# Kernel tuning notes

Hardware: AMD Instinct MI355X
Metric: run time of the kernel (lower is better)

Reference implementation:

```python
import jax, jax.numpy as jnp
import numpy as np

N_NODES = 100000
N_EDGES = 1600000
D_IN = 32
D_OUT = 32


def setup_inputs() -> dict:
    key = jax.random.key(0)
    k1, k2, k3 = jax.random.split(key, 3)
    x = jax.random.normal(k1, (N_NODES, D_IN), dtype=jnp.float32)
    edge_index = jax.random.randint(k2, (2, N_EDGES), 0, N_NODES, dtype=jnp.int64)
    # nn.Linear weight: [out_channels, in_channels]
    W = jax.random.normal(k3, (D_OUT, D_IN), dtype=jnp.float32) * (1.0 / np.sqrt(D_IN))
    return {"x": x, "edge_index": edge_index, "W": W}


def reference(x, edge_index, W):
    src, dst = edge_index[0], edge_index[1]
    # gather source features and scatter-add to destination nodes
    agg = jax.ops.segment_sum(x[src], dst, num_segments=x.shape[0])  # [N, D_IN]
    # linear (no bias): agg @ W.T
    return agg @ W.T
```

## Files before the change

kernel.cpp:

```cpp
#include <hip/hip_runtime.h>

#define N_NODES 100000
#define N_EDGES 1600000
#define D 32
#define Q8 256.0f
#define INV_Q8 (1.0f / 256.0f)
#define ROWS_PER_BLOCK 64
#define XS_STRIDE 36
#define NTILES ((N_NODES + ROWS_PER_BLOCK - 1) / ROWS_PER_BLOCK)
#define POISON64 0xAAAAAAAAAAAAAAAAULL
#define POISON32 0xAAAAAAAAu

#define BKT_NODES 256
#define NB ((N_NODES + BKT_NODES - 1) / BKT_NODES)
#define CAPB 8192
#define EPB 4096
#define K1_EPT (EPB / 256)
#define K1_BLOCKS ((N_EDGES + EPB - 1) / EPB)
#define K2_THREADS 512
#define QCAP 2048
#define MAX_WPT 12

#define GCUR_OFF 0
#define BUF_OFF  4096
#define YPK_OFF  (BUF_OFF + (size_t)NB * CAPB * 4)
#define WS_NEEDED (YPK_OFF + (size_t)N_NODES * 8 * 8)

__device__ __forceinline__ void decode4(unsigned long long s, float* o) {
    short v0 = (short)(s & 0xFFFF);
    s = (s >> 16) + (unsigned long long)(v0 < 0 ? 1 : 0);
    short v1 = (short)(s & 0xFFFF);
    s = (s >> 16) + (unsigned long long)(v1 < 0 ? 1 : 0);
    short v2 = (short)(s & 0xFFFF);
    s = (s >> 16) + (unsigned long long)(v2 < 0 ? 1 : 0);
    short v3 = (short)(s & 0xFFFF);
    o[0] = (float)v0 * INV_Q8;
    o[1] = (float)v1 * INV_Q8;
    o[2] = (float)v2 * INV_Q8;
    o[3] = (float)v3 * INV_Q8;
}

__global__ __launch_bounds__(256) void gcn_pack_bucket_kernel(
    const float4* __restrict__ x4,
    const float* __restrict__ W,
    const int* __restrict__ src,
    const int* __restrict__ dst,
    unsigned long long* __restrict__ ypk,
    unsigned int* __restrict__ gcur,
    unsigned int* __restrict__ buf) {
    __shared__ float xs[ROWS_PER_BLOCK * XS_STRIDE];
    __shared__ float Wt[D * D];
    __shared__ unsigned int cnt[NB];
    __shared__ unsigned int base[NB];
    int t = threadIdx.x;
    int b = blockIdx.x;

    if (b < NTILES) {
#pragma unroll
        for (int i = t; i < D * D; i += 256) {
            int o = i >> 5, k = i & 31;
            Wt[k * D + o] = W[i];
        }
        int row0 = b * ROWS_PER_BLOCK;
        int r = t >> 2;
        int c = t & 3;
        int grow = row0 + r;
        if (grow < N_NODES) {
            float4 v0 = x4[(size_t)grow * 8 + c * 2];
            float4 v1 = x4[(size_t)grow * 8 + c * 2 + 1];
            float* dp = &xs[r * XS_STRIDE + c * 8];
            dp[0] = v0.x; dp[1] = v0.y; dp[2] = v0.z; dp[3] = v0.w;
            dp[4] = v1.x; dp[5] = v1.y; dp[6] = v1.z; dp[7] = v1.w;
        }
        __syncthreads();
        if (grow >= N_NODES) return;

        int q = t & 3;
        float acc[8];
#pragma unroll
        for (int j = 0; j < 8; ++j) acc[j] = 0.f;
#pragma unroll
        for (int k = 0; k < D; ++k) {
            float v = xs[r * XS_STRIDE + k];
#pragma unroll
            for (int j = 0; j < 8; ++j) acc[j] += v * Wt[k * D + q * 8 + j];
        }
        long long a[8];
#pragma unroll
        for (int j = 0; j < 8; ++j)
            a[j] = (long long)__float2int_rn(acc[j] * Q8);
        unsigned long long p0 = (unsigned long long)(
            a[0] + (a[1] << 16) + (a[2] << 32) + (a[3] << 48));
        unsigned long long p1 = (unsigned long long)(
            a[4] + (a[5] << 16) + (a[6] << 32) + (a[7] << 48));
        ulonglong2* op = (ulonglong2*)(ypk + (size_t)grow * 8 + q * 2);
        *op = make_ulonglong2(p0, p1);
        return;
    }

    for (int j = t; j < NB; j += 256) cnt[j] = 0;
    __syncthreads();

    int e0 = (b - NTILES) * EPB;
    int s[K1_EPT], bkt[K1_EPT];
    unsigned int rank[K1_EPT], word[K1_EPT];
    bool ok[K1_EPT];
#pragma unroll
    for (int i = 0; i < K1_EPT; ++i) {
        int e = e0 + i * 256 + t;
        ok[i] = e < N_EDGES;
        int dd = 0;
        if (ok[i]) { s[i] = src[e]; dd = dst[e]; }
        bkt[i] = dd >> 8;
        word[i] = (unsigned int)s[i] | ((unsigned int)(dd & 255) << 17);
    }
#pragma unroll
    for (int i = 0; i < K1_EPT; ++i)
        if (ok[i]) rank[i] = atomicAdd(&cnt[bkt[i]], 1u);
    __syncthreads();

    for (int j = t; j < NB; j += 256) {
        unsigned int c = cnt[j];
        base[j] = c ? (atomicAdd(&gcur[j], c) - POISON32) : 0u;
    }
    __syncthreads();

#pragma unroll
    for (int i = 0; i < K1_EPT; ++i) {
        if (ok[i]) {
            unsigned int idx = base[bkt[i]] + rank[i];
            if (idx < CAPB)
                buf[(size_t)bkt[i] * CAPB + idx] = word[i];
        }
    }
}

__global__ __launch_bounds__(K2_THREADS) void gcn_sort_agg_kernel(
    const unsigned int* __restrict__ gcur,
    const unsigned int* __restrict__ buf,
    const unsigned long long* __restrict__ ypk,
    float* __restrict__ out) {
    __shared__ unsigned int sorted[QCAP];
    __shared__ unsigned int cnt[64];
    __shared__ unsigned int pfx[65];
    int t = threadIdx.x;
    int bq = blockIdx.x;
    int b = bq >> 2;
    int q = bq & 3;

    if (t < 64) cnt[t] = 0;
    __syncthreads();

    unsigned int cntb = gcur[b] - POISON32;
    if (cntb > 6144u) cntb = 6144u;
    const unsigned int* bb = buf + (size_t)b * CAPB;

    unsigned int w[MAX_WPT], rk[MAX_WPT];
    bool ok[MAX_WPT];
#pragma unroll
    for (int i = 0; i < MAX_WPT; ++i) {
        unsigned int g = (unsigned int)t + (unsigned int)i * K2_THREADS;
        ok[i] = (g < cntb);
        w[i] = ok[i] ? bb[g] : 0u;
        ok[i] = ok[i] && (((w[i] >> 23) & 3u) == (unsigned int)q);
    }
#pragma unroll
    for (int i = 0; i < MAX_WPT; ++i)
        if (ok[i]) rk[i] = atomicAdd(&cnt[(w[i] >> 17) & 63u], 1u);
    __syncthreads();

    if (t < 64) {
        unsigned int c = cnt[t];
        unsigned int v = c;
#pragma unroll
        for (int off = 1; off < 64; off <<= 1) {
            unsigned int u = __shfl_up(v, off, 64);
            if (t >= off) v += u;
        }
        pfx[t] = v - c;
        if (t == 63) pfx[64] = v;
    }
    __syncthreads();

#pragma unroll
    for (int i = 0; i < MAX_WPT; ++i) {
        if (ok[i]) {
            unsigned int idx = pfx[(w[i] >> 17) & 63u] + rk[i];
            if (idx < QCAP) sorted[idx] = w[i];
        }
    }
    __syncthreads();

    int r = t >> 3;
    int f4 = t & 7;
    unsigned int beg = pfx[r];
    unsigned int end = pfx[r + 1];
    unsigned long long sum = 0;
    unsigned int k = beg;
    for (; k + 8 <= end; k += 8) {
        unsigned int w0 = sorted[k],     w1 = sorted[k + 1];
        unsigned int w2 = sorted[k + 2], w3 = sorted[k + 3];
        unsigned int w4 = sorted[k + 4], w5 = sorted[k + 5];
        unsigned int w6 = sorted[k + 6], w7 = sorted[k + 7];
        unsigned long long y0 = ypk[(size_t)(w0 & 0x1FFFF) * 8 + f4];
        unsigned long long y1 = ypk[(size_t)(w1 & 0x1FFFF) * 8 + f4];
        unsigned long long y2 = ypk[(size_t)(w2 & 0x1FFFF) * 8 + f4];
        unsigned long long y3 = ypk[(size_t)(w3 & 0x1FFFF) * 8 + f4];
        unsigned long long y4 = ypk[(size_t)(w4 & 0x1FFFF) * 8 + f4];
        unsigned long long y5 = ypk[(size_t)(w5 & 0x1FFFF) * 8 + f4];
        unsigned long long y6 = ypk[(size_t)(w6 & 0x1FFFF) * 8 + f4];
        unsigned long long y7 = ypk[(size_t)(w7 & 0x1FFFF) * 8 + f4];
        sum += (y0 + y1) + (y2 + y3) + ((y4 + y5) + (y6 + y7));
    }
    for (; k < end; ++k)
        sum += ypk[(size_t)(sorted[k] & 0x1FFFF) * 8 + f4];

    int grow = (b << 8) + (q << 6) + r;
    if (grow < N_NODES) {
        float o4[4];
        decode4(sum, o4);
        *(float4*)(out + (size_t)grow * D + f4 * 4) =
            make_float4(o4[0], o4[1], o4[2], o4[3]);
    }
}


__global__ __launch_bounds__(256) void gcn_scatter_q_kernel(
    const int* __restrict__ src,
    const int* __restrict__ dst,
    const float4* __restrict__ x4,
    unsigned long long* __restrict__ agg) {
    int gid = blockIdx.x * 256 + threadIdx.x;
    int e = gid >> 3;
    int f4 = gid & 7;
    if (e >= N_EDGES) return;
    int s = src[e];
    int dd = dst[e];
    float4 v = x4[(size_t)s * 8 + f4];
    long long a0 = (long long)__float2int_rn(v.x * Q8);
    long long a1 = (long long)__float2int_rn(v.y * Q8);
    long long a2 = (long long)__float2int_rn(v.z * Q8);
    long long a3 = (long long)__float2int_rn(v.w * Q8);
    unsigned long long p =
        (unsigned long long)(a0 + (a1 << 16) + (a2 << 32) + (a3 << 48));
    atomicAdd(&agg[(size_t)dd * 8 + f4], p);
}

__global__ __launch_bounds__(256) void gcn_matmul_kernel(
    const unsigned long long* __restrict__ agg,
    const float* __restrict__ W,
    float* __restrict__ out) {
    __shared__ float xs[ROWS_PER_BLOCK * XS_STRIDE];
    __shared__ float Wt[D * D];
    int t = threadIdx.x;
    int b = blockIdx.x;

#pragma unroll
    for (int i = t; i < D * D; i += 256) {
        int o = i >> 5, k = i & 31;
        Wt[k * D + o] = W[i];
    }

    int row0 = b * ROWS_PER_BLOCK;
    {
        int r = t >> 2;
        int c = t & 3;
        int grow = row0 + r;
        if (grow < N_NODES) {
            const unsigned long long* rp = agg + (size_t)grow * 8 + c * 2;
            unsigned long long s0 = rp[0] - POISON64;
            unsigned long long s1 = rp[1] - POISON64;
            float* dstp = &xs[r * XS_STRIDE + c * 8];
            decode4(s0, dstp);
            decode4(s1, dstp + 4);
        }
    }
    __syncthreads();

    int r = t >> 2;
    int q = t & 3;
    int grow = row0 + r;
    if (grow >= N_NODES) return;

    float acc8[8];
#pragma unroll
    for (int j = 0; j < 8; ++j) acc8[j] = 0.f;
#pragma unroll
    for (int k = 0; k < D; ++k) {
        float v = xs[r * XS_STRIDE + k];
#pragma unroll
        for (int j = 0; j < 8; ++j) acc8[j] += v * Wt[k * D + q * 8 + j];
    }
    float4* op = (float4*)(out + (size_t)grow * D + q * 8);
    op[0] = make_float4(acc8[0], acc8[1], acc8[2], acc8[3]);
    op[1] = make_float4(acc8[4], acc8[5], acc8[6], acc8[7]);
}

extern "C" void kernel_launch(void* const* d_in, const int* in_sizes, int n_in,
                              void* d_out, int out_size, void* d_ws, size_t ws_size,
                              hipStream_t stream) {
    const float* x = (const float*)d_in[0];
    const int* edge_index = (const int*)d_in[1];
    const float* W = (const float*)d_in[2];
    float* out = (float*)d_out;

    const int* src = edge_index;
    const int* dst = edge_index + N_EDGES;

    char* ws = (char*)d_ws;

    if (ws_size >= WS_NEEDED) {
        unsigned int* gcur = (unsigned int*)(ws + GCUR_OFF);
        unsigned int* buf = (unsigned int*)(ws + BUF_OFF);
        unsigned long long* ypk = (unsigned long long*)(ws + YPK_OFF);

        gcn_pack_bucket_kernel<<<NTILES + K1_BLOCKS, 256, 0, stream>>>(
            (const float4*)x, W, src, dst, ypk, gcur, buf);
        gcn_sort_agg_kernel<<<NB * 4, K2_THREADS, 0, stream>>>(
            gcur, buf, ypk, out);
    } else {
        unsigned long long* agg = (unsigned long long*)ws;
        gcn_scatter_q_kernel<<<(N_EDGES * 8) / 256, 256, 0, stream>>>(
            src, dst, (const float4*)x, agg);
        gcn_matmul_kernel<<<NTILES, 256, 0, stream>>>(agg, W, out);
    }
}
```

Baseline: 119.6 us.

## Fuse bucketing, transform and sort-aggregate into one cooperative kernel with grid sync

Merges the pack/bucket kernel and the sort-aggregate kernel into a single cooperative launch of 512 persistent blocks. Each block first buckets a slice of edges, then computes and quantizes rows of x·W into a grid-strided set of tiles, and after a grid-wide sync it loops over the bucket quarters to sort and aggregate. This removes the second kernel launch and the inter-kernel gap. The cost is a grid barrier, fewer resident blocks with persistent loops, and a higher register and shared-memory footprint per block. The old two-kernel path remains as a fallback if the cooperative launch fails.

```diff
diff --git a/kernel.cpp b/kernel.cpp
--- a/kernel.cpp
+++ b/kernel.cpp
@@ -1,4 +1,7 @@
 #include <hip/hip_runtime.h>
+#include <hip/hip_cooperative_groups.h>
+
+namespace cg = cooperative_groups;
 
 #define N_NODES 100000
 #define N_EDGES 1600000
@@ -20,6 +23,10 @@
 #define K2_THREADS 512
 #define QCAP 2048
 #define MAX_WPT 12
+
+#define FUSE_BLOCKS 512
+#define FUSE_THREADS 512
+#define EPT2 (EPB / FUSE_THREADS)
 
 #define GCUR_OFF 0
 #define BUF_OFF  4096
@@ -40,120 +47,13 @@
     o[3] = (float)v3 * INV_Q8;
 }
 
-__global__ __launch_bounds__(256) void gcn_pack_bucket_kernel(
-    const float4* __restrict__ x4,
-    const float* __restrict__ W,
-    const int* __restrict__ src,
-    const int* __restrict__ dst,
-    unsigned long long* __restrict__ ypk,
-    unsigned int* __restrict__ gcur,
-    unsigned int* __restrict__ buf) {
-    __shared__ float xs[ROWS_PER_BLOCK * XS_STRIDE];
-    __shared__ float Wt[D * D];
-    __shared__ unsigned int cnt[NB];
-    __shared__ unsigned int base[NB];
+__device__ __forceinline__ void quarter_sort_agg(
+    int b, int q, unsigned int cntb, const unsigned int* __restrict__ bb,
+    const unsigned long long* __restrict__ ypk, float* __restrict__ out,
+    unsigned int* sorted, unsigned int* cnt, unsigned int* pfx) {
     int t = threadIdx.x;
-    int b = blockIdx.x;
-
-    if (b < NTILES) {
-#pragma unroll
-        for (int i = t; i < D * D; i += 256) {
-            int o = i >> 5, k = i & 31;
-            Wt[k * D + o] = W[i];
-        }
-        int row0 = b * ROWS_PER_BLOCK;
-        int r = t >> 2;
-        int c = t & 3;
-        int grow = row0 + r;
-        if (grow < N_NODES) {
-            float4 v0 = x4[(size_t)grow * 8 + c * 2];
-            float4 v1 = x4[(size_t)grow * 8 + c * 2 + 1];
-            float* dp = &xs[r * XS_STRIDE + c * 8];
-            dp[0] = v0.x; dp[1] = v0.y; dp[2] = v0.z; dp[3] = v0.w;
-            dp[4] = v1.x; dp[5] = v1.y; dp[6] = v1.z; dp[7] = v1.w;
-        }
-        __syncthreads();
-        if (grow >= N_NODES) return;
-
-        int q = t & 3;
-        float acc[8];
-#pragma unroll
-        for (int j = 0; j < 8; ++j) acc[j] = 0.f;
-#pragma unroll
-        for (int k = 0; k < D; ++k) {
-            float v = xs[r * XS_STRIDE + k];
-#pragma unroll
-            for (int j = 0; j < 8; ++j) acc[j] += v * Wt[k * D + q * 8 + j];
-        }
-        long long a[8];
-#pragma unroll
-        for (int j = 0; j < 8; ++j)
-            a[j] = (long long)__float2int_rn(acc[j] * Q8);
-        unsigned long long p0 = (unsigned long long)(
-            a[0] + (a[1] << 16) + (a[2] << 32) + (a[3] << 48));
-        unsigned long long p1 = (unsigned long long)(
-            a[4] + (a[5] << 16) + (a[6] << 32) + (a[7] << 48));
-        ulonglong2* op = (ulonglong2*)(ypk + (size_t)grow * 8 + q * 2);
-        *op = make_ulonglong2(p0, p1);
-        return;
-    }
-
-    for (int j = t; j < NB; j += 256) cnt[j] = 0;
-    __syncthreads();
-
-    int e0 = (b - NTILES) * EPB;
-    int s[K1_EPT], bkt[K1_EPT];
-    unsigned int rank[K1_EPT], word[K1_EPT];
-    bool ok[K1_EPT];
-#pragma unroll
-    for (int i = 0; i < K1_EPT; ++i) {
-        int e = e0 + i * 256 + t;
-        ok[i] = e < N_EDGES;
-        int dd = 0;
-        if (ok[i]) { s[i] = src[e]; dd = dst[e]; }
-        bkt[i] = dd >> 8;
-        word[i] = (unsigned int)s[i] | ((unsigned int)(dd & 255) << 17);
-    }
-#pragma unroll
-    for (int i = 0; i < K1_EPT; ++i)
-        if (ok[i]) rank[i] = atomicAdd(&cnt[bkt[i]], 1u);
-    __syncthreads();
-
-    for (int j = t; j < NB; j += 256) {
-        unsigned int c = cnt[j];
-        base[j] = c ? (atomicAdd(&gcur[j], c) - POISON32) : 0u;
-    }
-    __syncthreads();
-
-#pragma unroll
-    for (int i = 0; i < K1_EPT; ++i) {
-        if (ok[i]) {
-            unsigned int idx = base[bkt[i]] + rank[i];
-            if (idx < CAPB)
-                buf[(size_t)bkt[i] * CAPB + idx] = word[i];
-        }
-    }
-}
-
-__global__ __launch_bounds__(K2_THREADS) void gcn_sort_agg_kernel(
-    const unsigned int* __restrict__ gcur,
-    const unsigned int* __restrict__ buf,
-    const unsigned long long* __restrict__ ypk,
-    float* __restrict__ out) {
-    __shared__ unsigned int sorted[QCAP];
-    __shared__ unsigned int cnt[64];
-    __shared__ unsigned int pfx[65];
-    int t = threadIdx.x;
-    int bq = blockIdx.x;
-    int b = bq >> 2;
-    int q = bq & 3;
-
     if (t < 64) cnt[t] = 0;
     __syncthreads();
-
-    unsigned int cntb = gcur[b] - POISON32;
-    if (cntb > 6144u) cntb = 6144u;
-    const unsigned int* bb = buf + (size_t)b * CAPB;
 
     unsigned int w[MAX_WPT], rk[MAX_WPT];
     bool ok[MAX_WPT];
@@ -222,6 +122,221 @@
         *(float4*)(out + (size_t)grow * D + f4 * 4) =
             make_float4(o4[0], o4[1], o4[2], o4[3]);
     }
+    __syncthreads();
+}
+
+__global__ __launch_bounds__(FUSE_THREADS, 4) void gcn_fused_kernel(
+    const float4* __restrict__ x4, const float* __restrict__ W,
+    const int* __restrict__ src, const int* __restrict__ dst,
+    unsigned long long* __restrict__ ypk, unsigned int* __restrict__ gcur,
+    unsigned int* __restrict__ buf, float* __restrict__ out) {
+    __shared__ float Wt[D * D];
+    __shared__ float xs[64 * XS_STRIDE];
+    __shared__ unsigned int cnt1[NB];
+    __shared__ unsigned int base1[NB];
+    __shared__ unsigned int sorted[QCAP];
+    __shared__ unsigned int cnt2[64];
+    __shared__ unsigned int pfx[65];
+    int t = threadIdx.x;
+    int b = blockIdx.x;
+    int nblk = gridDim.x;
+
+    for (int i = t; i < D * D; i += FUSE_THREADS) {
+        int o = i >> 5, k = i & 31;
+        Wt[k * D + o] = W[i];
+    }
+
+    if (b < K1_BLOCKS) {
+        for (int j = t; j < NB; j += FUSE_THREADS) cnt1[j] = 0;
+        __syncthreads();
+        int e0 = b * EPB;
+        int s[EPT2], bkt[EPT2];
+        unsigned int rank[EPT2], word[EPT2];
+        bool ok[EPT2];
+#pragma unroll
+        for (int i = 0; i < EPT2; ++i) {
+            int e = e0 + i * FUSE_THREADS + t;
+            ok[i] = e < N_EDGES;
+            int dd = 0;
+            if (ok[i]) { s[i] = src[e]; dd = dst[e]; }
+            bkt[i] = dd >> 8;
+            word[i] = (unsigned int)s[i] | ((unsigned int)(dd & 255) << 17);
+        }
+#pragma unroll
+        for (int i = 0; i < EPT2; ++i)
+            if (ok[i]) rank[i] = atomicAdd(&cnt1[bkt[i]], 1u);
+        __syncthreads();
+        if (t < NB) {
+            unsigned int c = cnt1[t];
+            base1[t] = c ? (atomicAdd(&gcur[t], c) - POISON32) : 0u;
+        }
+        __syncthreads();
+#pragma unroll
+        for (int i = 0; i < EPT2; ++i) {
+            if (ok[i]) {
+                unsigned int idx = base1[bkt[i]] + rank[i];
+                if (idx < CAPB) buf[(size_t)bkt[i] * CAPB + idx] = word[i];
+            }
+        }
+    }
+    __syncthreads();
+
+    int tb = (b >= K1_BLOCKS) ? (b - K1_BLOCKS) : (b + (nblk - K1_BLOCKS));
+    for (int tile = tb; tile < NTILES; tile += nblk) {
+        int row0 = tile * ROWS_PER_BLOCK;
+        int r = t >> 3;
+        int h = t & 7;
+        int grow = row0 + r;
+        if (grow < N_NODES) {
+            float4 v = x4[(size_t)grow * 8 + h];
+            float* dp = &xs[r * XS_STRIDE + h * 4];
+            dp[0] = v.x; dp[1] = v.y; dp[2] = v.z; dp[3] = v.w;
+        }
+        __syncthreads();
+        if (grow < N_NODES) {
+            float acc[4];
+#pragma unroll
+            for (int j = 0; j < 4; ++j) acc[j] = 0.f;
+#pragma unroll
+            for (int k = 0; k < D; ++k) {
+                float v = xs[r * XS_STRIDE + k];
+#pragma unroll
+                for (int j = 0; j < 4; ++j) acc[j] += v * Wt[k * D + h * 4 + j];
+            }
+            long long a0 = (long long)__float2int_rn(acc[0] * Q8);
+            long long a1 = (long long)__float2int_rn(acc[1] * Q8);
+            long long a2 = (long long)__float2int_rn(acc[2] * Q8);
+            long long a3 = (long long)__float2int_rn(acc[3] * Q8);
+            ypk[(size_t)grow * 8 + h] = (unsigned long long)(
+                a0 + (a1 << 16) + (a2 << 32) + (a3 << 48));
+        }
+        __syncthreads();
+    }
+
+    cg::this_grid().sync();
+
+    for (int qq = b; qq < NB * 4; qq += nblk) {
+        int bb_ = qq >> 2, q = qq & 3;
+        unsigned int cntb = __hip_atomic_load(&gcur[bb_], __ATOMIC_RELAXED,
+                                              __HIP_MEMORY_SCOPE_AGENT) -
+                            POISON32;
+        if (cntb > 6144u) cntb = 6144u;
+        quarter_sort_agg(bb_, q, cntb, buf + (size_t)bb_ * CAPB, ypk, out,
+                         sorted, cnt2, pfx);
+    }
+}
+
+
+__global__ __launch_bounds__(256) void gcn_pack_bucket_kernel(
+    const float4* __restrict__ x4,
+    const float* __restrict__ W,
+    const int* __restrict__ src,
+    const int* __restrict__ dst,
+    unsigned long long* __restrict__ ypk,
+    unsigned int* __restrict__ gcur,
+    unsigned int* __restrict__ buf) {
+    __shared__ float xs[ROWS_PER_BLOCK * XS_STRIDE];
+    __shared__ float Wt[D * D];
+    __shared__ unsigned int cnt[NB];
+    __shared__ unsigned int base[NB];
+    int t = threadIdx.x;
+    int b = blockIdx.x;
+
+    if (b < NTILES) {
+#pragma unroll
+        for (int i = t; i < D * D; i += 256) {
+            int o = i >> 5, k = i & 31;
+            Wt[k * D + o] = W[i];
+        }
+        int row0 = b * ROWS_PER_BLOCK;
+        int r = t >> 2;
+        int c = t & 3;
+        int grow = row0 + r;
+        if (grow < N_NODES) {
+            float4 v0 = x4[(size_t)grow * 8 + c * 2];
+            float4 v1 = x4[(size_t)grow * 8 + c * 2 + 1];
+            float* dp = &xs[r * XS_STRIDE + c * 8];
+            dp[0] = v0.x; dp[1] = v0.y; dp[2] = v0.z; dp[3] = v0.w;
+            dp[4] = v1.x; dp[5] = v1.y; dp[6] = v1.z; dp[7] = v1.w;
+        }
+        __syncthreads();
+        if (grow >= N_NODES) return;
+
+        int q = t & 3;
+        float acc[8];
+#pragma unroll
+        for (int j = 0; j < 8; ++j) acc[j] = 0.f;
+#pragma unroll
+        for (int k = 0; k < D; ++k) {
+            float v = xs[r * XS_STRIDE + k];
+#pragma unroll
+            for (int j = 0; j < 8; ++j) acc[j] += v * Wt[k * D + q * 8 + j];
+        }
+        long long a[8];
+#pragma unroll
+        for (int j = 0; j < 8; ++j)
+            a[j] = (long long)__float2int_rn(acc[j] * Q8);
+        unsigned long long p0 = (unsigned long long)(
+            a[0] + (a[1] << 16) + (a[2] << 32) + (a[3] << 48));
+        unsigned long long p1 = (unsigned long long)(
+            a[4] + (a[5] << 16) + (a[6] << 32) + (a[7] << 48));
+        ulonglong2* op = (ulonglong2*)(ypk + (size_t)grow * 8 + q * 2);
+        *op = make_ulonglong2(p0, p1);
+        return;
+    }
+
+    for (int j = t; j < NB; j += 256) cnt[j] = 0;
+    __syncthreads();
+
+    int e0 = (b - NTILES) * EPB;
+    int s[K1_EPT], bkt[K1_EPT];
+    unsigned int rank[K1_EPT], word[K1_EPT];
+    bool ok[K1_EPT];
+#pragma unroll
+    for (int i = 0; i < K1_EPT; ++i) {
+        int e = e0 + i * 256 + t;
+        ok[i] = e < N_EDGES;
+        int dd = 0;
+        if (ok[i]) { s[i] = src[e]; dd = dst[e]; }
+        bkt[i] = dd >> 8;
+        word[i] = (unsigned int)s[i] | ((unsigned int)(dd & 255) << 17);
+    }
+#pragma unroll
+    for (int i = 0; i < K1_EPT; ++i)
+        if (ok[i]) rank[i] = atomicAdd(&cnt[bkt[i]], 1u);
+    __syncthreads();
+
+    for (int j = t; j < NB; j += 256) {
+        unsigned int c = cnt[j];
+        base[j] = c ? (atomicAdd(&gcur[j], c) - POISON32) : 0u;
+    }
+    __syncthreads();
+
+#pragma unroll
+    for (int i = 0; i < K1_EPT; ++i) {
+        if (ok[i]) {
+            unsigned int idx = base[bkt[i]] + rank[i];
+            if (idx < CAPB)
+                buf[(size_t)bkt[i] * CAPB + idx] = word[i];
+        }
+    }
+}
+
+__global__ __launch_bounds__(K2_THREADS) void gcn_sort_agg_kernel(
+    const unsigned int* __restrict__ gcur,
+    const unsigned int* __restrict__ buf,
+    const unsigned long long* __restrict__ ypk,
+    float* __restrict__ out) {
+    __shared__ unsigned int sorted[QCAP];
+    __shared__ unsigned int cnt[64];
+    __shared__ unsigned int pfx[65];
+    int bq = blockIdx.x;
+    int b = bq >> 2;
+    int q = bq & 3;
+    unsigned int cntb = gcur[b] - POISON32;
+    if (cntb > 6144u) cntb = 6144u;
+    quarter_sort_agg(b, q, cntb, buf + (size_t)b * CAPB, ypk, out,
+                     sorted, cnt, pfx);
 }
 
 
@@ -314,10 +429,27 @@
         unsigned int* buf = (unsigned int*)(ws + BUF_OFF);
         unsigned long long* ypk = (unsigned long long*)(ws + YPK_OFF);
 
-        gcn_pack_bucket_kernel<<<NTILES + K1_BLOCKS, 256, 0, stream>>>(
-            (const float4*)x, W, src, dst, ypk, gcur, buf);
-        gcn_sort_agg_kernel<<<NB * 4, K2_THREADS, 0, stream>>>(
-            gcur, buf, ypk, out);
+        const float4* x4p = (const float4*)x;
+        const float* Wp = W;
+        const int* srcp = src;
+        const int* dstp = dst;
+        unsigned long long* ypkp = ypk;
+        unsigned int* gcurp = gcur;
+        unsigned int* bufp = buf;
+        float* outp = out;
+        void* kargs[] = {(void*)&x4p,  (void*)&Wp,    (void*)&srcp,
+                         (void*)&dstp, (void*)&ypkp,  (void*)&gcurp,
+                         (void*)&bufp, (void*)&outp};
+        hipError_t cerr = hipLaunchCooperativeKernel(
+            (const void*)gcn_fused_kernel, dim3(FUSE_BLOCKS),
+            dim3(FUSE_THREADS), kargs, 0, stream);
+        if (cerr != hipSuccess) {
+            (void)hipGetLastError();
+            gcn_pack_bucket_kernel<<<NTILES + K1_BLOCKS, 256, 0, stream>>>(
+                (const float4*)x, W, src, dst, ypk, gcur, buf);
+            gcn_sort_agg_kernel<<<NB * 4, K2_THREADS, 0, stream>>>(
+                gcur, buf, ypk, out);
+        }
     } else {
         unsigned long long* agg = (unsigned long long*)ws;
         gcn_scatter_q_kernel<<<(N_EDGES * 8) / 256, 256, 0, stream>>>(
```

New measurement: 209.1 us. +74.9%, slower.

## Split packed projected features into two planes and aggregate each half separately

Applied to the files above, without the earlier changes.

The packed fixed-point projected features are stored as two feature planes of 16 columns each instead of one 32-column row. Aggregation now runs as two launches, one per plane, and each block covers 128 destination rows with 4 threads per row. Each pass gathers from a table half the size, which should improve cache hit rates on the random source gathers. The cost is one extra launch, and every bucket has to be re-read and re-sorted in each pass.

```diff
diff --git a/kernel.cpp b/kernel.cpp
--- a/kernel.cpp
+++ b/kernel.cpp
@@ -18,13 +18,14 @@
 #define K1_EPT (EPB / 256)
 #define K1_BLOCKS ((N_EDGES + EPB - 1) / EPB)
 #define K2_THREADS 512
-#define QCAP 2048
+#define HCAP 4096
 #define MAX_WPT 12
 
 #define GCUR_OFF 0
 #define BUF_OFF  4096
 #define YPK_OFF  (BUF_OFF + (size_t)NB * CAPB * 4)
-#define WS_NEEDED (YPK_OFF + (size_t)N_NODES * 8 * 8)
+#define PLANE_U64 ((size_t)N_NODES * 4)
+#define WS_NEEDED (YPK_OFF + 2 * PLANE_U64 * 8)
 
 __device__ __forceinline__ void decode4(unsigned long long s, float* o) {
     short v0 = (short)(s & 0xFFFF);
@@ -45,7 +46,8 @@
     const float* __restrict__ W,
     const int* __restrict__ src,
     const int* __restrict__ dst,
-    unsigned long long* __restrict__ ypk,
+    unsigned long long* __restrict__ ylo,
+    unsigned long long* __restrict__ yhi,
     unsigned int* __restrict__ gcur,
     unsigned int* __restrict__ buf) {
     __shared__ float xs[ROWS_PER_BLOCK * XS_STRIDE];
@@ -93,7 +95,9 @@
             a[0] + (a[1] << 16) + (a[2] << 32) + (a[3] << 48));
         unsigned long long p1 = (unsigned long long)(
             a[4] + (a[5] << 16) + (a[6] << 32) + (a[7] << 48));
-        ulonglong2* op = (ulonglong2*)(ypk + (size_t)grow * 8 + q * 2);
+        unsigned long long* plane = (q < 2) ? ylo : yhi;
+        ulonglong2* op =
+            (ulonglong2*)(plane + (size_t)grow * 4 + (q & 1) * 2);
         *op = make_ulonglong2(p0, p1);
         return;
     }
@@ -135,20 +139,22 @@
     }
 }
 
-__global__ __launch_bounds__(K2_THREADS) void gcn_sort_agg_kernel(
+template <int PLANE>
+__global__ __launch_bounds__(K2_THREADS) void gcn_sort_agg_half_kernel(
     const unsigned int* __restrict__ gcur,
     const unsigned int* __restrict__ buf,
-    const unsigned long long* __restrict__ ypk,
+    const unsigned long long* __restrict__ ypl,
     float* __restrict__ out) {
-    __shared__ unsigned int sorted[QCAP];
-    __shared__ unsigned int cnt[64];
-    __shared__ unsigned int pfx[65];
+    __shared__ unsigned int sorted[HCAP];
+    __shared__ unsigned int cnt[128];
+    __shared__ unsigned int pfx[129];
+    __shared__ unsigned int wtot[2];
     int t = threadIdx.x;
-    int bq = blockIdx.x;
-    int b = bq >> 2;
-    int q = bq & 3;
-
-    if (t < 64) cnt[t] = 0;
+    int bh = blockIdx.x;
+    int b = bh >> 1;
+    int h = bh & 1;
+
+    if (t < 128) cnt[t] = 0;
     __syncthreads();
 
     unsigned int cntb = gcur[b] - POISON32;
@@ -162,37 +168,43 @@
         unsigned int g = (unsigned int)t + (unsigned int)i * K2_THREADS;
         ok[i] = (g < cntb);
         w[i] = ok[i] ? bb[g] : 0u;
-        ok[i] = ok[i] && (((w[i] >> 23) & 3u) == (unsigned int)q);
+        ok[i] = ok[i] && (((w[i] >> 24) & 1u) == (unsigned int)h);
     }
 #pragma unroll
     for (int i = 0; i < MAX_WPT; ++i)
-        if (ok[i]) rk[i] = atomicAdd(&cnt[(w[i] >> 17) & 63u], 1u);
-    __syncthreads();
-
-    if (t < 64) {
-        unsigned int c = cnt[t];
-        unsigned int v = c;
+        if (ok[i]) rk[i] = atomicAdd(&cnt[(w[i] >> 17) & 127u], 1u);
+    __syncthreads();
+
+    unsigned int v = 0, c = 0;
+    if (t < 128) {
+        c = cnt[t];
+        v = c;
 #pragma unroll
         for (int off = 1; off < 64; off <<= 1) {
             unsigned int u = __shfl_up(v, off, 64);
-            if (t >= off) v += u;
-        }
-        pfx[t] = v - c;
-        if (t == 63) pfx[64] = v;
+            if ((t & 63) >= off) v += u;
+        }
+        if ((t & 63) == 63) wtot[t >> 6] = v;
+    }
+    __syncthreads();
+    if (t < 128) {
+        unsigned int add = (t >= 64) ? wtot[0] : 0u;
+        pfx[t] = v - c + add;
+        if (t == 127) pfx[128] = v + add;
     }
     __syncthreads();
 
 #pragma unroll
     for (int i = 0; i < MAX_WPT; ++i) {
         if (ok[i]) {
-            unsigned int idx = pfx[(w[i] >> 17) & 63u] + rk[i];
-            if (idx < QCAP) sorted[idx] = w[i];
-        }
-    }
-    __syncthreads();
-
-    int r = t >> 3;
-    int f4 = t & 7;
+            unsigned int idx = pfx[(w[i] >> 17) & 127u] + rk[i];
+            if (idx < HCAP) sorted[idx] = w[i];
+        }
+    }
+    __syncthreads();
+
+    int r = t >> 2;
+    int f4 = t & 3;
     unsigned int beg = pfx[r];
     unsigned int end = pfx[r + 1];
     unsigned long long sum = 0;
@@ -202,24 +214,24 @@
         unsigned int w2 = sorted[k + 2], w3 = sorted[k + 3];
         unsigned int w4 = sorted[k + 4], w5 = sorted[k + 5];
         unsigned int w6 = sorted[k + 6], w7 = sorted[k + 7];
-        unsigned long long y0 = ypk[(size_t)(w0 & 0x1FFFF) * 8 + f4];
-        unsigned long long y1 = ypk[(size_t)(w1 & 0x1FFFF) * 8 + f4];
-        unsigned long long y2 = ypk[(size_t)(w2 & 0x1FFFF) * 8 + f4];
-        unsigned long long y3 = ypk[(size_t)(w3 & 0x1FFFF) * 8 + f4];
-        unsigned long long y4 = ypk[(size_t)(w4 & 0x1FFFF) * 8 + f4];
-        unsigned long long y5 = ypk[(size_t)(w5 & 0x1FFFF) * 8 + f4];
-        unsigned long long y6 = ypk[(size_t)(w6 & 0x1FFFF) * 8 + f4];
-        unsigned long long y7 = ypk[(size_t)(w7 & 0x1FFFF) * 8 + f4];
+        unsigned long long y0 = ypl[(size_t)(w0 & 0x1FFFF) * 4 + f4];
+        unsigned long long y1 = ypl[(size_t)(w1 & 0x1FFFF) * 4 + f4];
+        unsigned long long y2 = ypl[(size_t)(w2 & 0x1FFFF) * 4 + f4];
+        unsigned long long y3 = ypl[(size_t)(w3 & 0x1FFFF) * 4 + f4];
+        unsigned long long y4 = ypl[(size_t)(w4 & 0x1FFFF) * 4 + f4];
+        unsigned long long y5 = ypl[(size_t)(w5 & 0x1FFFF) * 4 + f4];
+        unsigned long long y6 = ypl[(size_t)(w6 & 0x1FFFF) * 4 + f4];
+        unsigned long long y7 = ypl[(size_t)(w7 & 0x1FFFF) * 4 + f4];
         sum += (y0 + y1) + (y2 + y3) + ((y4 + y5) + (y6 + y7));
     }
     for (; k < end; ++k)
-        sum += ypk[(size_t)(sorted[k] & 0x1FFFF) * 8 + f4];
-
-    int grow = (b << 8) + (q << 6) + r;
+        sum += ypl[(size_t)(sorted[k] & 0x1FFFF) * 4 + f4];
+
+    int grow = (b << 8) + (h << 7) + r;
     if (grow < N_NODES) {
         float o4[4];
         decode4(sum, o4);
-        *(float4*)(out + (size_t)grow * D + f4 * 4) =
+        *(float4*)(out + (size_t)grow * D + PLANE * 16 + f4 * 4) =
             make_float4(o4[0], o4[1], o4[2], o4[3]);
     }
 }
@@ -312,12 +324,15 @@
     if (ws_size >= WS_NEEDED) {
         unsigned int* gcur = (unsigned int*)(ws + GCUR_OFF);
         unsigned int* buf = (unsigned int*)(ws + BUF_OFF);
-        unsigned long long* ypk = (unsigned long long*)(ws + YPK_OFF);
+        unsigned long long* ylo = (unsigned long long*)(ws + YPK_OFF);
+        unsigned long long* yhi = ylo + PLANE_U64;
 
         gcn_pack_bucket_kernel<<<NTILES + K1_BLOCKS, 256, 0, stream>>>(
-            (const float4*)x, W, src, dst, ypk, gcur, buf);
-        gcn_sort_agg_kernel<<<NB * 4, K2_THREADS, 0, stream>>>(
-            gcur, buf, ypk, out);
+            (const float4*)x, W, src, dst, ylo, yhi, gcur, buf);
+        gcn_sort_agg_half_kernel<0><<<NB * 2, K2_THREADS, 0, stream>>>(
+            gcur, buf, ylo, out);
+        gcn_sort_agg_half_kernel<1><<<NB * 2, K2_THREADS, 0, stream>>>(
+            gcur, buf, yhi, out);
     } else {
         unsigned long long* agg = (unsigned long long*)ws;
         gcn_scatter_q_kernel<<<(N_EDGES * 8) / 256, 256, 0, stream>>>(
```

Result: slower. 130.1 us (+8.8%).
